# Optimization experiments

Measured on AMD Instinct MI355X. Metric: run time of the kernel, lower is better.

The kernel has to match this reference:

```python
import jax, jax.numpy as jnp
import numpy as np

B, N, DIM = 4, 4096, 512
HEADS, DH = 8, 64          # dim_head = dim // 8
M = 256                    # num_landmarks = dim // 2
ITERS = 6                  # pinv iterations
K = 33                     # residual depthwise conv kernel
INNER = HEADS * DH


def setup_inputs() -> dict:
    key = jax.random.key(0)
    ks = jax.random.split(key, 7)
    return {
        "x": jax.random.normal(ks[0], (B, N, DIM), jnp.float32),
        "norm_w": 1.0 + 0.02 * jax.random.normal(ks[1], (DIM,), jnp.float32),
        "norm_b": 0.02 * jax.random.normal(ks[2], (DIM,), jnp.float32),
        "w_qkv": jax.random.normal(ks[3], (DIM, 3 * INNER), jnp.float32) / np.sqrt(DIM),
        "w_out": jax.random.normal(ks[4], (INNER, DIM), jnp.float32) / np.sqrt(INNER),
        "b_out": 0.02 * jax.random.normal(ks[5], (DIM,), jnp.float32),
        "res_w": jax.random.normal(ks[6], (HEADS, 1, K, 1), jnp.float32) / np.sqrt(K),
    }


def _moore_penrose_pinv(x, iters):
    # iterative Newton-Schulz pseudoinverse, as in lucidrains nystrom-attention
    abs_x = jnp.abs(x)
    col = abs_x.sum(-1)
    row = abs_x.sum(-2)
    z = jnp.swapaxes(x, -1, -2) / (jnp.max(col) * jnp.max(row))
    I = jnp.eye(x.shape[-1], dtype=x.dtype)
    for _ in range(iters):
        xz = x @ z
        z = 0.25 * z @ (13.0 * I - xz @ (15.0 * I - xz @ (7.0 * I - xz)))
    return z


def reference(x, norm_w, norm_b, w_qkv, w_out, b_out, res_w):
    # LayerNorm (eps=1e-5, torch default)
    mu = x.mean(-1, keepdims=True)
    var = ((x - mu) ** 2).mean(-1, keepdims=True)
    xn = (x - mu) / jnp.sqrt(var + 1e-5) * norm_w + norm_b

    qkv = xn @ w_qkv                               # [B,N,3*INNER]
    q, k, v = jnp.split(qkv, 3, axis=-1)
    to_heads = lambda t: t.reshape(B, N, HEADS, DH).transpose(0, 2, 1, 3)  # [B,H,N,D]
    q, k, v = to_heads(q), to_heads(k), to_heads(v)
    q = q * (DH ** -0.5)

    # landmarks: mean over consecutive blocks of l = N // M tokens
    l = N // M
    q_l = q.reshape(B, HEADS, M, l, DH).mean(3)    # [B,H,M,D]
    k_l = k.reshape(B, HEADS, M, l, DH).mean(3)

    sim1 = jnp.einsum('bhid,bhjd->bhij', q, k_l)   # [B,H,N,M]
    sim2 = jnp.einsum('bhid,bhjd->bhij', q_l, k_l) # [B,H,M,M]
    sim3 = jnp.einsum('bhid,bhjd->bhij', q_l, k)   # [B,H,M,N]
    a1 = jax.nn.softmax(sim1, -1)
    a2 = jax.nn.softmax(sim2, -1)
    a3 = jax.nn.softmax(sim3, -1)

    a2_inv = _moore_penrose_pinv(a2, ITERS)
    out = (a1 @ a2_inv) @ (a3 @ v)                 # [B,H,N,D]

    # residual depthwise conv over sequence dim (Conv2d(h,h,(33,1),groups=h))
    out = out + jax.lax.conv_general_dilated(
        v, res_w, (1, 1), ((K // 2, K // 2), (0, 0)),
        feature_group_count=HEADS,
        dimension_numbers=('NCHW', 'OIHW', 'NCHW'))

    out = out.transpose(0, 2, 1, 3).reshape(B, N, INNER)
    out = out @ w_out + b_out                      # to_out (dropout inactive at eval)
    return x + out                                 # TransLayer residual
```

## Files before the change

kernel.cpp:

```cpp
#include <hip/hip_runtime.h>
#include <math.h>

typedef unsigned short u16;
typedef short s16x8 __attribute__((ext_vector_type(8)));
typedef float f32x4 __attribute__((ext_vector_type(4)));

#define MFMA16(a, b, c) __builtin_amdgcn_mfma_f32_16x16x32_bf16((a), (b), (c), 0, 0, 0)

__device__ __forceinline__ u16 f2b(float f) {
  unsigned u = __float_as_uint(f);
  unsigned r = (u + 0x7fff + ((u >> 16) & 1)) >> 16;
  return (u16)r;
}
__device__ __forceinline__ float b2f(u16 h) { return __uint_as_float(((unsigned)h) << 16); }

__global__ __launch_bounds__(256) void prep_kernel(const float* __restrict__ x, const float* __restrict__ w,
    const float* __restrict__ b, u16* __restrict__ xn,
    const float* __restrict__ Wq, u16* __restrict__ WqT,
    const float* __restrict__ Wo, u16* __restrict__ WoT,
    unsigned* __restrict__ scal) {
  int bI = blockIdx.x;
  int t = threadIdx.x;
  if (bI == 0 && t == 0) { scal[0] = 0u; scal[1] = 0u; }
  if (bI < 16384) {
    int row = bI;
    const float* xr = x + (size_t)row * 512;
    float v0 = xr[t], v1 = xr[t + 256];
    float s = v0 + v1, ss = v0*v0 + v1*v1;
    for (int o = 32; o > 0; o >>= 1) { s += __shfl_down(s, o); ss += __shfl_down(ss, o); }
    __shared__ float ls[4], lss[4];
    int wid = t >> 6, lane = t & 63;
    if (lane == 0) { ls[wid] = s; lss[wid] = ss; }
    __syncthreads();
    float tot  = ls[0]+ls[1]+ls[2]+ls[3];
    float tot2 = lss[0]+lss[1]+lss[2]+lss[3];
    float mean = tot * (1.f/512);
    float var  = tot2 * (1.f/512) - mean*mean;
    float inv = rsqrtf(var + 1e-5f);
    u16* xo = xn + (size_t)row * 512;
    xo[t]     = f2b((v0-mean)*inv*w[t]     + b[t]);
    xo[t+256] = f2b((v1-mean)*inv*w[t+256] + b[t+256]);
  } else if (bI < 16384 + 3072) {
    int idx = (bI - 16384)*256 + t;
    int r = idx / 1536, c = idx - r*1536;
    WqT[(size_t)c*512 + r] = f2b(Wq[idx]);
  } else {
    int idx = (bI - 19456)*256 + t;
    int r = idx >> 9, c = idx & 511;
    WoT[(size_t)c*512 + r] = f2b(Wo[idx]);
  }
}

__global__ __launch_bounds__(256) void vtrans(const u16* __restrict__ v, u16* __restrict__ vT) {
  __shared__ u16 tile[64][72];
  int bh = blockIdx.y, n0 = blockIdx.x * 64;
  int t = threadIdx.x;
  const u16* vb = v + ((size_t)bh*4096 + n0)*64;
  #pragma unroll
  for (int p = 0; p < 2; p++) {
    int c = t + p*256;
    int r = c >> 3, col = (c & 7)*8;
    *(uint4*)&tile[r][col] = *(const uint4*)&vb[(size_t)r*64 + col];
  }
  __syncthreads();
  #pragma unroll
  for (int p = 0; p < 2; p++) {
    int c = t + p*256;
    int d = c >> 3, ncol = (c & 7)*8;
    u16 tmp[8];
    #pragma unroll
    for (int j = 0; j < 8; j++) tmp[j] = tile[ncol + j][d];
    *(uint4*)&vT[((size_t)bh*64 + d)*4096 + n0 + ncol] = *(uint4*)tmp;
  }
}

__device__ __forceinline__ void gemm128_pf(const u16* __restrict__ A, const u16* __restrict__ BT,
    int K, int ldA, int ldBT, int row0, int col0, u16* As, u16* Bs, f32x4 acc[4][4]) {
  int t = threadIdx.x, lane = t & 63, wid = t >> 6;
  int wr = (wid >> 1) * 64, wc = (wid & 1) * 64;
  int lr = lane & 15, lg = lane >> 4;
  int sr = t >> 2, sc = (t & 3) * 8;
  const u16* Ar0 = A  + (size_t)(row0 + sr)*ldA + sc;
  const u16* Ar1 = A  + (size_t)(row0 + sr + 64)*ldA + sc;
  const u16* Br0 = BT + (size_t)(col0 + sr)*ldBT + sc;
  const u16* Br1 = BT + (size_t)(col0 + sr + 64)*ldBT + sc;
  uint4 pa0 = *(const uint4*)Ar0, pa1 = *(const uint4*)Ar1;
  uint4 pb0 = *(const uint4*)Br0, pb1 = *(const uint4*)Br1;
  for (int k0 = 0; k0 < K; k0 += 32) {
    __syncthreads();
    *(uint4*)&As[sr*40 + sc]        = pa0;
    *(uint4*)&As[(sr + 64)*40 + sc] = pa1;
    *(uint4*)&Bs[sr*40 + sc]        = pb0;
    *(uint4*)&Bs[(sr + 64)*40 + sc] = pb1;
    __syncthreads();
    if (k0 + 32 < K) {
      pa0 = *(const uint4*)(Ar0 + k0 + 32);
      pa1 = *(const uint4*)(Ar1 + k0 + 32);
      pb0 = *(const uint4*)(Br0 + k0 + 32);
      pb1 = *(const uint4*)(Br1 + k0 + 32);
    }
    s16x8 af[4], bf[4];
    #pragma unroll
    for (int f = 0; f < 4; f++) {
      af[f] = *(s16x8*)&As[(wr + f*16 + lr)*40 + lg*8];
      bf[f] = *(s16x8*)&Bs[(wc + f*16 + lr)*40 + lg*8];
    }
    #pragma unroll
    for (int i = 0; i < 4; i++)
// ... 96 lines not shown
          if (part == 0) ql[dst] = f2b(s * (0.125f/16.f));
          else           kl[dst] = f2b(s * (1.f/16.f));
        }
      }
    }
  }
}

__global__ __launch_bounds__(256, 4) void out_mfma(const u16* __restrict__ outh, const u16* __restrict__ wT,
    const float* __restrict__ bo, const float* __restrict__ x, float* __restrict__ out) {
  __shared__ u16 As[128*40], Bs[128*40];
  f32x4 acc[4][4];
  #pragma unroll
  for (int i = 0; i < 4; i++)
    #pragma unroll
    for (int j = 0; j < 4; j++) acc[i][j] = (f32x4)0.f;
  int bI = blockIdx.x;
  int job = (bI & 7)*64 + (bI >> 3);
  int row0 = (job / 4) * 128, col0 = (job % 4) * 128;
  gemm128_pf(outh, wT, 512, 512, 512, row0, col0, As, Bs, acc);
  int t = threadIdx.x, lane = t & 63, wid = t >> 6, lr = lane & 15, lg = lane >> 4;
  int wr = (wid >> 1)*64, wc = (wid & 1)*64;
  #pragma unroll
  for (int i = 0; i < 4; i++)
    #pragma unroll
    for (int j = 0; j < 4; j++)
      #pragma unroll
      for (int r = 0; r < 4; r++) {
        int row = row0 + wr + i*16 + lg*4 + r;
        int col = col0 + wc + j*16 + lr;
        size_t idx = (size_t)row*512 + col;
        out[idx] = x[idx] + acc[i][j][r] + bo[col];
      }
}

__global__ __launch_bounds__(256) void pinv_s1(const u16* __restrict__ a2h, const u16* __restrict__ zcT,
    u16* __restrict__ xz, u16* __restrict__ xzT, u16* __restrict__ e1T) {
  __shared__ u16 As[64*72], Bs[64*72];
  size_t bb = (size_t)blockIdx.z << 16;
  f32x4 acc[2][2];
  #pragma unroll
  for (int i = 0; i < 2; i++) { acc[i][0] = (f32x4)0.f; acc[i][1] = (f32x4)0.f; }
  int row0 = blockIdx.y*64, col0 = blockIdx.x*64;
  gemm64_pf(a2h + bb, zcT + bb, row0, col0, As, Bs, acc);
  int t = threadIdx.x, lane = t & 63, wid = t >> 6, lr = lane & 15, lg = lane >> 4;
  int wr = (wid >> 1)*32, wc = (wid & 1)*32;
  #pragma unroll
  for (int i = 0; i < 2; i++)
    #pragma unroll
    for (int j = 0; j < 2; j++)
      #pragma unroll
      for (int r = 0; r < 4; r++) {
        int row = row0 + wr + i*16 + lg*4 + r;
        int col = col0 + wc + j*16 + lr;
        float c = acc[i][j][r];
        xz [bb + (size_t)row*256 + col] = f2b(c);
        xzT[bb + (size_t)col*256 + row] = f2b(c);
        e1T[bb + (size_t)col*256 + row] = f2b((row == col ? 7.f : 0.f) - c);
      }
}

__global__ __launch_bounds__(256) void pinv_s2(const u16* __restrict__ xz, const u16* __restrict__ e1T,
    const u16* __restrict__ zc, const u16* __restrict__ xzT,
    u16* __restrict__ e2T, u16* __restrict__ W) {
  __shared__ u16 As[64*72], Bs[64*72];
  int bz = blockIdx.z;
// ... 71 lines not shown
    __syncthreads();
    *(uint4*)&As[sr*40 + sc] = pa;
    *(uint4*)&Bs[sr*40 + sc] = pb;
    __syncthreads();
    if (k0 + 32 < K) {
      pa = *(const uint4*)(Arow + k0 + 32);
      pb = *(const uint4*)(Brow + k0 + 32);
    }
    s16x8 af[2], bf[2];
    #pragma unroll
    for (int f = 0; f < 2; f++) {
      af[f] = *(s16x8*)&As[(wr + f*16 + lr)*40 + lg*8];
      bf[f] = *(s16x8*)&Bs[(wc + f*16 + lr)*40 + lg*8];
    }
    #pragma unroll
    for (int i = 0; i < 2; i++)
      #pragma unroll
      for (int j = 0; j < 2; j++)
        acc[i][j] = MFMA16(af[i], bf[j], acc[i][j]);
  }
  size_t cb = (size_t)batch*M*N;
  #pragma unroll
  for (int i = 0; i < 2; i++)
    #pragma unroll
    for (int j = 0; j < 2; j++)
      #pragma unroll
      for (int r = 0; r < 4; r++) {
        int row = row0 + wr + i*16 + lg*4 + r;
        int col = col0 + wc + j*16 + lr;
        CT[cb + (size_t)col*M + row] = f2b(acc[i][j][r]);
      }
}

__global__ __launch_bounds__(256, 4) void sim2_mfma(const u16* __restrict__ ql, const u16* __restrict__ kl,
    float* __restrict__ a2, u16* __restrict__ a2h, float* __restrict__ pcs) {
  __shared__ u16 Qs[64*72];
  __shared__ u16 Ks2[256*72];
  __shared__ float wcol[4*256];
  int rq = blockIdx.x, bh = blockIdx.y;
  int t = threadIdx.x, lane = t & 63, wid = t >> 6, lr = lane & 15, lg = lane >> 4;
  #pragma unroll
  for (int p = 0; p < 2; p++) {
    int c = t + p*256;
    int r = c >> 3, col = (c & 7)*8;
    *(uint4*)&Qs[r*72 + col] = *(const uint4*)&ql[((size_t)bh*256 + rq*64 + r)*64 + col];
  }
  #pragma unroll
  for (int p = 0; p < 8; p++) {
    int c = t + p*256;
    int r = c >> 3, col = (c & 7)*8;
    *(uint4*)&Ks2[r*72 + col] = *(const uint4*)&kl[((size_t)bh*256 + r)*64 + col];
  }
  __syncthreads();
  float colp[16];
  #pragma unroll
  for (int cf = 0; cf < 16; cf++) colp[cf] = 0.f;
  int rbase = wid*16;
  s16x8 a0 = *(s16x8*)&Qs[(rbase + lr)*72 + lg*8];
  s16x8 a1 = *(s16x8*)&Qs[(rbase + lr)*72 + 32 + lg*8];
  f32x4 sf[16];
  #pragma unroll
  for (int cf = 0; cf < 16; cf++) {
    s16x8 b0 = *(s16x8*)&Ks2[(cf*16 + lr)*72 + lg*8];
    s16x8 b1 = *(s16x8*)&Ks2[(cf*16 + lr)*72 + 32 + lg*8];
    sf[cf] = MFMA16(a1, b1, MFMA16(a0, b0, (f32x4)0.f));
  }
  #pragma unroll
  for (int r = 0; r < 4; r++) {
    float mx = -3e38f;
    #pragma unroll
    for (int cf = 0; cf < 16; cf++) mx = fmaxf(mx, sf[cf][r]);
    #pragma unroll
    for (int o = 1; o < 16; o <<= 1) mx = fmaxf(mx, __shfl_xor(mx, o));
    float sum = 0.f;
    #pragma unroll
    for (int cf = 0; cf < 16; cf++) { sf[cf][r] = __expf(sf[cf][r] - mx); sum += sf[cf][r]; }
    #pragma unroll
    for (int o = 1; o < 16; o <<= 1) sum += __shfl_xor(sum, o);
    float inv = 1.f / sum;
    int row = rq*64 + rbase + lg*4 + r;
    size_t base = (size_t)bh*65536 + (size_t)row*256;
    #pragma unroll
    for (int cf = 0; cf < 16; cf++) {
      float pp = sf[cf][r] * inv;
      a2[base + cf*16 + lr] = pp;
      a2h[base + cf*16 + lr] = f2b(pp);
      colp[cf] += pp;
    }
  }
  #pragma unroll
  for (int cf = 0; cf < 16; cf++) {
    colp[cf] += __shfl_xor(colp[cf], 16);
    colp[cf] += __shfl_xor(colp[cf], 32);
  }
  if (lg == 0) {
    #pragma unroll
    for (int cf = 0; cf < 16; cf++) wcol[wid*256 + cf*16 + lr] = colp[cf];
  }
  __syncthreads();
  pcs[((size_t)bh*4 + rq)*256 + t] = wcol[t] + wcol[256 + t] + wcol[512 + t] + wcol[768 + t];
}

__global__ __launch_bounds__(256) void colmax_kernel(const float* __restrict__ pcs, unsigned* __restrict__ scal) {
  __shared__ float red[256];
  int bh = blockIdx.x, t = threadIdx.x;
  size_t b4 = (size_t)bh*4*256;
  red[t] = pcs[b4 + t] + pcs[b4 + 256 + t] + pcs[b4 + 512 + t] + pcs[b4 + 768 + t];
  __syncthreads();
  for (int o = 128; o > 0; o >>= 1) {
    if (t < o) red[t] = fmaxf(red[t], red[t+o]);
    __syncthreads();
  }
  if (t == 0) atomicMax(scal + 1, __float_as_uint(red[0]));
}

__global__ __launch_bounds__(256) void flash_part(const u16* __restrict__ Q, const u16* __restrict__ Kg,
    const u16* __restrict__ VT, u16* __restrict__ po, float* __restrict__ pl) {
  __shared__ u16 Ks[64*72];
  __shared__ u16 Vs[64*72];
  __shared__ u16 Ps[4*16*72];
  int ch = blockIdx.x, qg = blockIdx.y, bh = blockIdx.z;
  int t = threadIdx.x, lane = t & 63, wid = t >> 6, lr = lane & 15, lg = lane >> 4;
  const u16* Qb  = Q  + ((size_t)bh*256)*64;
  const u16* Kb  = Kg + ((size_t)bh*4096 + ch*512)*64;
  const u16* VTb = VT + ((size_t)bh*64)*4096 + ch*512;
  s16x8 aq[2][2];
  #pragma unroll
  for (int qq = 0; qq < 2; qq++) {
    int qrow = (qg*2 + qq)*64 + wid*16 + lr;
    aq[qq][0] = *(const s16x8*)&Qb[(size_t)qrow*64 + lg*8];
    aq[qq][1] = *(const s16x8*)&Qb[(size_t)qrow*64 + 32 + lg*8];
  }
  f32x4 oacc[2][4];
  f32x4 lacc[2];
  #pragma unroll
  for (int qq = 0; qq < 2; qq++) {
    lacc[qq] = (f32x4)0.f;
    #pragma unroll
    for (int f = 0; f < 4; f++) oacc[qq][f] = (f32x4)0.f;
  }
  u16* Pw = Ps + wid*16*72;
  uint4 pk[2], pv[2];
  #pragma unroll
  for (int p = 0; p < 2; p++) {
    int c = t + p*256; int r = c >> 3, cc = (c & 7)*8;
    pk[p] = *(const uint4*)&Kb[(size_t)r*64 + cc];
    pv[p] = *(const uint4*)&VTb[(size_t)r*4096 + cc];
  }
  for (int k0 = 0; k0 < 512; k0 += 64) {
    __syncthreads();
    #pragma unroll
    for (int p = 0; p < 2; p++) {
      int c = t + p*256; int r = c >> 3, cc = (c & 7)*8;
      *(uint4*)&Ks[r*72 + cc] = pk[p];
      *(uint4*)&Vs[r*72 + cc] = pv[p];
    }
    __syncthreads();
    if (k0 + 64 < 512) {
      #pragma unroll
      for (int p = 0; p < 2; p++) {
        int c = t + p*256; int r = c >> 3, cc = (c & 7)*8;
        pk[p] = *(const uint4*)&Kb[(size_t)(k0 + 64 + r)*64 + cc];
        pv[p] = *(const uint4*)&VTb[(size_t)r*4096 + k0 + 64 + cc];
      }
    }
    #pragma unroll
    for (int qq = 0; qq < 2; qq++) {
      f32x4 sf[4];
      #pragma unroll
      for (int f = 0; f < 4; f++) {
        s16x8 b0 = *(s16x8*)&Ks[(f*16 + lr)*72 + lg*8];
        s16x8 b1 = *(s16x8*)&Ks[(f*16 + lr)*72 + 32 + lg*8];
        f32x4 s = (f32x4)0.f;
        s = MFMA16(aq[qq][0], b0, s);
        s = MFMA16(aq[qq][1], b1, s);
        sf[f] = s;
      }
      #pragma unroll
      for (int r = 0; r < 4; r++) {
        #pragma unroll
        for (int f = 0; f < 4; f++) {
          float pv2 = __expf(sf[f][r] - 8.f);
          lacc[qq][r] += pv2;
          Pw[(lg*4 + r)*72 + f*16 + lr] = f2b(pv2);
        }
      }
      #pragma unroll
      for (int ks = 0; ks < 2; ks++) {
        s16x8 ap = *(s16x8*)&Pw[lr*72 + ks*32 + lg*8];
        #pragma unroll
        for (int df = 0; df < 4; df++) {
          s16x8 bv = *(s16x8*)&Vs[(df*16 + lr)*72 + ks*32 + lg*8];
          oacc[qq][df] = MFMA16(ap, bv, oacc[qq][df]);
        }
      }
    }
  }
  #pragma unroll
  for (int qq = 0; qq < 2; qq++) {
    #pragma unroll
    for (int r = 0; r < 4; r++) {
      float s = lacc[qq][r];
      #pragma unroll
      for (int o = 1; o < 16; o <<= 1) s += __shfl_xor(s, o);
      lacc[qq][r] = s;
    }
  }
  #pragma unroll
  for (int qq = 0; qq < 2; qq++) {
    int pidx = (bh*4 + qg*2 + qq)*8 + ch;
    #pragma unroll
    for (int r = 0; r < 4; r++) {
      int lrow = wid*16 + lg*4 + r;
      if (lr == 0) pl[pidx*64 + lrow] = lacc[qq][r];
      uint2 pw2;
      pw2.x = (unsigned)f2b(oacc[qq][0][r]) | ((unsigned)f2b(oacc[qq][1][r]) << 16);
      pw2.y = (unsigned)f2b(oacc[qq][2][r]) | ((unsigned)f2b(oacc[qq][3][r]) << 16);
      *(uint2*)&po[((size_t)pidx*64 + lrow)*64 + lr*4] = pw2;
    }
  }
}

__global__ __launch_bounds__(256) void merge_z0(const u16* __restrict__ po,
    const float* __restrict__ pl, u16* __restrict__ a3vT,
    const float* __restrict__ a2, const unsigned* __restrict__ scal,
    u16* __restrict__ zA, u16* __restrict__ zAT) {
  __shared__ u16 tile[64*72];
  int bI = blockIdx.x;
  int t = threadIdx.x;
  if (bI < 128) {
    int qt = bI & 3, bh = bI >> 2;
    int lrow = t & 63, dg = t >> 6;
    int pbase = (bh*4 + qt)*8;
    float L = 0.f;
    #pragma unroll
    for (int ch = 0; ch < 8; ch++) L += pl[(pbase+ch)*64 + lrow];
    float Oacc[16];
    #pragma unroll
    for (int ss = 0; ss < 16; ss++) Oacc[ss] = 0.f;
    #pragma unroll
    for (int ch = 0; ch < 8; ch++) {
      const u16* pr = &po[(((size_t)(pbase+ch)*64 + lrow)*64) + dg*16];
      uint4 v0 = *(const uint4*)pr;
      uint4 v1 = *(const uint4*)(pr + 8);
      unsigned arr[8] = {v0.x, v0.y, v0.z, v0.w, v1.x, v1.y, v1.z, v1.w};
      #pragma unroll
      for (int jj = 0; jj < 8; jj++) {
        Oacc[jj*2]   += b2f((u16)(arr[jj] & 0xffff));
        Oacc[jj*2+1] += b2f((u16)(arr[jj] >> 16));
      }
    }
    float Linv = 1.f / L;
    #pragma unroll
    for (int ss = 0; ss < 16; ss++) {
      int s = dg*16 + ss;
      int c = ((s & 3) << 4) | (s >> 2);
      tile[c*72 + lrow] = f2b(Oacc[ss] * Linv);
    }
    __syncthreads();
    #pragma unroll
    for (int p = 0; p < 2; p++) {
      int idx = t + p*256;
      int d = idx >> 3, seg = idx & 7;
      u16 tmp[8];
      #pragma unroll
      for (int j = 0; j < 8; j++) tmp[j] = tile[d*72 + seg*8 + j];
      *(uint4*)&a3vT[((size_t)bh*64 + d)*256 + qt*64 + seg*8] = *(uint4*)tmp;
    }
  } else {
    size_t idx = (size_t)(bI - 128)*256 + t;
    float inv = 1.f / __uint_as_float(scal[1]);
    size_t bh = idx >> 16; int rem = (int)(idx & 65535); int i = rem >> 8, j = rem & 255;
    zA[idx]  = f2b(a2[(bh<<16) + ((size_t)j<<8) + i] * inv);
    zAT[idx] = f2b(a2[idx] * inv);
  }
}

__global__ __launch_bounds__(256, 4) void flash_a1(const u16* __restrict__ Q, const u16* __restrict__ Kl,
    const u16* __restrict__ W2T, u16* __restrict__ outh) {
  __shared__ u16 Ks[64*72];
  __shared__ u16 Vs[64*264];
  __shared__ u16 Ps[4*16*264];
  int bh = blockIdx.y;
  int q0 = blockIdx.x * 64;
  int t = threadIdx.x, lane = t & 63, wid = t >> 6, lr = lane & 15, lg = lane >> 4;
  const u16* Qb = Q + ((size_t)bh*4096)*64;
  #pragma unroll
  for (int p = 0; p < 8; p++) {
    int c = t + p*256; int r = c >> 5, col = (c & 31)*8;
    *(uint4*)&Vs[r*264 + col] = *(const uint4*)&W2T[((size_t)bh*64 + r)*256 + col];
  }
  int qrow = q0 + wid*16 + lr;
  s16x8 aq0 = *(const s16x8*)&Qb[(size_t)qrow*64 + lg*8];
  s16x8 aq1 = *(const s16x8*)&Qb[(size_t)qrow*64 + 32 + lg*8];
  f32x4 sf[16];
  #pragma unroll
  for (int f = 0; f < 16; f++) sf[f] = (f32x4)0.f;
  #pragma unroll
  for (int kt = 0; kt < 4; kt++) {
    __syncthreads();
    #pragma unroll
    for (int p = 0; p < 2; p++) {
      int c = t + p*256; int r = c >> 3, cc = (c & 7)*8;
      *(uint4*)&Ks[r*72 + cc] = *(const uint4*)&Kl[((size_t)bh*256 + kt*64 + r)*64 + cc];
    }
    __syncthreads();
    #pragma unroll
    for (int f2 = 0; f2 < 4; f2++) {
      s16x8 b0 = *(s16x8*)&Ks[(f2*16 + lr)*72 + lg*8];
      s16x8 b1 = *(s16x8*)&Ks[(f2*16 + lr)*72 + 32 + lg*8];
// ... 4 lines not shown
  float linv[4];
  #pragma unroll
  for (int r = 0; r < 4; r++) {
    float sum = 0.f;
    #pragma unroll
    for (int f = 0; f < 16; f++) {
      float pv = __expf(sf[f][r] - 8.f);
      sum += pv;
      Pw[(lg*4 + r)*264 + f*16 + lr] = f2b(pv);
    }
    #pragma unroll
    for (int o = 1; o < 16; o <<= 1) sum += __shfl_xor(sum, o);
    linv[r] = 1.f / sum;
  }
  f32x4 oacc[4];
  #pragma unroll
  for (int f = 0; f < 4; f++) oacc[f] = (f32x4)0.f;
  #pragma unroll
  for (int ks = 0; ks < 8; ks++) {
    s16x8 ap = *(s16x8*)&Pw[lr*264 + ks*32 + lg*8];
    #pragma unroll
    for (int df = 0; df < 4; df++) {
      s16x8 bv = *(s16x8*)&Vs[(df*16 + lr)*264 + ks*32 + lg*8];
      oacc[df] = MFMA16(ap, bv, oacc[df]);
    }
  }
  int b = bh >> 3, h = bh & 7;
  #pragma unroll
  for (int df = 0; df < 4; df++)
    #pragma unroll
    for (int r = 0; r < 4; r++) {
      int lrow = wid*16 + lg*4 + r;
      int col = df*16 + lr;
      outh[((size_t)(b*4096 + q0 + lrow))*512 + h*64 + col] = f2b(oacc[df][r] * linv[r]);
    }
}

__global__ __launch_bounds__(256) void conv_lds(const u16* __restrict__ v, const float* __restrict__ rw,
                                                u16* __restrict__ outh) {
  __shared__ u16 tile[160*72];
  __shared__ float wsm[33];
  int bh = blockIdx.y;
  int n0 = blockIdx.x * 128;
  int b = bh >> 3, h = bh & 7;
  int t = threadIdx.x;
  if (t < 33) wsm[t] = rw[h*33 + t];
  const u16* vb = v + ((size_t)bh*4096)*64;
  #pragma unroll
  for (int p = 0; p < 5; p++) {
    int c = t + p*256;
    int r = c >> 3, col = (c & 7)*8;
    int nn = n0 - 16 + r;
    uint4 val = make_uint4(0u,0u,0u,0u);
    if (nn >= 0 && nn < 4096) val = *(const uint4*)&vb[(size_t)nn*64 + col];
    *(uint4*)&tile[r*72 + col] = val;
  }
  __syncthreads();
  int d8 = (t & 7) * 8;
  int r0 = t >> 3;
  #pragma unroll
  for (int pass = 0; pass < 4; pass++) {
    int lrow = pass*32 + r0;
    float acc[8] = {};
    #pragma unroll
    for (int j = 0; j < 33; j++) {
      uint4 vv = *(uint4*)&tile[(lrow + j)*72 + d8];
      float w = wsm[j];
      acc[0] += b2f((u16)(vv.x & 0xffff)) * w;
      acc[1] += b2f((u16)(vv.x >> 16))    * w;
      acc[2] += b2f((u16)(vv.y & 0xffff)) * w;
      acc[3] += b2f((u16)(vv.y >> 16))    * w;
      acc[4] += b2f((u16)(vv.z & 0xffff)) * w;
      acc[5] += b2f((u16)(vv.z >> 16))    * w;
      acc[6] += b2f((u16)(vv.w & 0xffff)) * w;
      acc[7] += b2f((u16)(vv.w >> 16))    * w;
    }
    size_t oi = ((size_t)(b*4096 + n0 + lrow))*512 + h*64 + d8;
    uint4 ov = *(uint4*)&outh[oi];
    uint4 nv;
    nv.x = (unsigned)f2b(b2f((u16)(ov.x & 0xffff)) + acc[0]) | ((unsigned)f2b(b2f((u16)(ov.x >> 16)) + acc[1]) << 16);
    nv.y = (unsigned)f2b(b2f((u16)(ov.y & 0xffff)) + acc[2]) | ((unsigned)f2b(b2f((u16)(ov.y >> 16)) + acc[3]) << 16);
    nv.z = (unsigned)f2b(b2f((u16)(ov.z & 0xffff)) + acc[4]) | ((unsigned)f2b(b2f((u16)(ov.z >> 16)) + acc[5]) << 16);
    nv.w = (unsigned)f2b(b2f((u16)(ov.w & 0xffff)) + acc[6]) | ((unsigned)f2b(b2f((u16)(ov.w >> 16)) + acc[7]) << 16);
    *(uint4*)&outh[oi] = nv;
  }
}

extern "C" void kernel_launch(void* const* d_in, const int* in_sizes, int n_in,
                              void* d_out, int out_size, void* d_ws, size_t ws_size,
                              hipStream_t stream) {
  const float* x      = (const float*)d_in[0];
  const float* norm_w = (const float*)d_in[1];
  const float* norm_b = (const float*)d_in[2];
  const float* w_qkv  = (const float*)d_in[3];
  const float* w_out  = (const float*)d_in[4];
  const float* b_out  = (const float*)d_in[5];
  const float* res_w  = (const float*)d_in[6];
  float* out = (float*)d_out;
  char* ws = (char*)d_ws;

  size_t off = 0;
  u16* xn    = (u16*)(ws + off); off += 16777216;
  u16* q     = (u16*)(ws + off); off += 16777216;
  u16* k     = (u16*)(ws + off); off += 16777216;
  u16* v     = (u16*)(ws + off); off += 16777216;
  u16* vT    = (u16*)(ws + off); off += 16777216;
  u16* ql    = (u16*)(ws + off); off += 1048576;
  u16* kl    = (u16*)(ws + off); off += 1048576;
  float* a2  = (float*)(ws + off); off += 8388608;
  u16* a2h   = (u16*)(ws + off); off += 4194304;
  u16* zA    = (u16*)(ws + off); off += 4194304;
  u16* zAT   = (u16*)(ws + off); off += 4194304;
  u16* zB    = (u16*)(ws + off); off += 4194304;
  u16* zBT   = (u16*)(ws + off); off += 4194304;
  u16* xz    = (u16*)(ws + off); off += 4194304;
  u16* xzT   = (u16*)(ws + off); off += 4194304;
  u16* e1T   = (u16*)(ws + off); off += 4194304;
  u16* e2T   = (u16*)(ws + off); off += 4194304;
  u16* Wm    = (u16*)(ws + off); off += 4194304;
  u16* a3vT  = (u16*)(ws + off); off += 1048576;
  u16* w2T   = (u16*)(ws + off); off += 1048576;
  u16* wqkvT = (u16*)(ws + off); off += 1572864;
  u16* woutT = (u16*)(ws + off); off += 524288;
  u16* outh  = (u16*)(ws + off); off += 16777216;
  u16* po    = (u16*)(ws + off); off += 8388608;
  float* pl  = (float*)(ws + off); off += 262144;
  float* pcs = (float*)(ws + off); off += 131072;
  unsigned* scal = (unsigned*)(ws + off); off += 8;

  prep_kernel<<<20480, 256, 0, stream>>>(x, norm_w, norm_b, xn, w_qkv, wqkvT, w_out, woutT, scal);
  qkv_mfma<<<1536, 256, 0, stream>>>(xn, wqkvT, q, k, v, ql, kl);
  vtrans<<<dim3(64, 32), 256, 0, stream>>>(v, vT);
  sim2_mfma<<<dim3(4, 32), 256, 0, stream>>>(ql, kl, a2, a2h, pcs);
  colmax_kernel<<<32, 256, 0, stream>>>(pcs, scal);
  flash_part<<<dim3(8, 2, 32), 256, 0, stream>>>(ql, k, vT, po, pl);
  merge_z0<<<8320, 256, 0, stream>>>(po, pl, a3vT, a2, scal, zA, zAT);

  u16 *zc = zA, *zcT = zAT, *zn = zB, *znT = zBT;
  for (int it = 0; it < 6; it++) {
    pinv_s1<<<dim3(4,4,32), 256, 0, stream>>>(a2h, zcT, xz, xzT, e1T);
    pinv_s2<<<dim3(4,4,64), 256, 0, stream>>>(xz, e1T, zc, xzT, e2T, Wm);
    pinv_s3<<<dim3(4,4,32), 256, 0, stream>>>(Wm, e2T, zc, zn, znT);
    u16* tp;
    tp = zc; zc = zn; zn = tp;
    tp = zcT; zcT = znT; znT = tp;
  }

  bmm64<<<dim3(1,4,32), 256, 0, stream>>>(zc, a3vT, w2T, 256, 64, 256);
  flash_a1<<<dim3(64, 32), 256, 0, stream>>>(q, kl, w2T, outh);
  conv_lds<<<dim3(32, 32), 256, 0, stream>>>(v, res_w, outh);
  out_mfma<<<512, 256, 0, stream>>>(outh, woutT, b_out, x, out);
}
```

Measured before the change: 397.6 us.

## Fuse vtrans, sim2 softmax and residual conv into one mid kernel

Three independent stages (landmark softmax sim2, V transpose, depthwise residual conv) now run as one kernel, with each block choosing its task from the block index. The conv result is written to outh first, and flash_a1 adds its attention output on top by read-modify-write, so the separate conv pass that reread outh goes away. The fp32 a2 buffer is removed and merge_z0 builds z0 from the bf16 a2h instead. This saves launches and memory traffic, at the cost of a slightly less precise initial z.

```diff
diff --git a/kernel.cpp b/kernel.cpp
--- a/kernel.cpp
+++ b/kernel.cpp
@@ -51,29 +51,6 @@
   }
 }
 
-__global__ __launch_bounds__(256) void vtrans(const u16* __restrict__ v, u16* __restrict__ vT) {
-  __shared__ u16 tile[64][72];
-  int bh = blockIdx.y, n0 = blockIdx.x * 64;
-  int t = threadIdx.x;
-  const u16* vb = v + ((size_t)bh*4096 + n0)*64;
-  #pragma unroll
-  for (int p = 0; p < 2; p++) {
-    int c = t + p*256;
-    int r = c >> 3, col = (c & 7)*8;
-    *(uint4*)&tile[r][col] = *(const uint4*)&vb[(size_t)r*64 + col];
-  }
-  __syncthreads();
-  #pragma unroll
-  for (int p = 0; p < 2; p++) {
-    int c = t + p*256;
-    int d = c >> 3, ncol = (c & 7)*8;
-    u16 tmp[8];
-    #pragma unroll
-    for (int j = 0; j < 8; j++) tmp[j] = tile[ncol + j][d];
-    *(uint4*)&vT[((size_t)bh*64 + d)*4096 + n0 + ncol] = *(uint4*)tmp;
-  }
-}
-
 __device__ __forceinline__ void gemm128_pf(const u16* __restrict__ A, const u16* __restrict__ BT,
     int K, int ldA, int ldBT, int row0, int col0, u16* As, u16* Bs, f32x4 acc[4][4]) {
   int t = threadIdx.x, lane = t & 63, wid = t >> 6;
@@ -236,6 +213,323 @@
         size_t idx = (size_t)row*512 + col;
         out[idx] = x[idx] + acc[i][j][r] + bo[col];
       }
+}
+
+__global__ __launch_bounds__(256) void mid_kernel(
+    const u16* __restrict__ v, u16* __restrict__ vT,
+    const u16* __restrict__ ql, const u16* __restrict__ kl,
+    u16* __restrict__ a2h, float* __restrict__ pcs,
+    const float* __restrict__ rw, u16* __restrict__ outh) {
+  __shared__ __align__(16) u16 smem[25600];
+  int bI = blockIdx.x;
+  int t = threadIdx.x;
+  if (bI < 128) {
+    int rq = bI & 3, bh = bI >> 2;
+    u16* Qs  = smem;
+    u16* Ks2 = smem + 4608;
+    float* wcol = (float*)(smem + 23040);
+    int lane = t & 63, wid = t >> 6, lr = lane & 15, lg = lane >> 4;
+    #pragma unroll
+    for (int p = 0; p < 2; p++) {
+      int c = t + p*256;
+      int r = c >> 3, col = (c & 7)*8;
+      *(uint4*)&Qs[r*72 + col] = *(const uint4*)&ql[((size_t)bh*256 + rq*64 + r)*64 + col];
+    }
+    #pragma unroll
+    for (int p = 0; p < 8; p++) {
+      int c = t + p*256;
+      int r = c >> 3, col = (c & 7)*8;
+      *(uint4*)&Ks2[r*72 + col] = *(const uint4*)&kl[((size_t)bh*256 + r)*64 + col];
+    }
+    __syncthreads();
+    float colp[16];
+    #pragma unroll
+    for (int cf = 0; cf < 16; cf++) colp[cf] = 0.f;
+    int rbase = wid*16;
+    s16x8 a0 = *(s16x8*)&Qs[(rbase + lr)*72 + lg*8];
+    s16x8 a1 = *(s16x8*)&Qs[(rbase + lr)*72 + 32 + lg*8];
+    f32x4 sf[16];
+    #pragma unroll
+    for (int cf = 0; cf < 16; cf++) {
+      s16x8 b0 = *(s16x8*)&Ks2[(cf*16 + lr)*72 + lg*8];
+      s16x8 b1 = *(s16x8*)&Ks2[(cf*16 + lr)*72 + 32 + lg*8];
+      sf[cf] = MFMA16(a1, b1, MFMA16(a0, b0, (f32x4)0.f));
+    }
+    #pragma unroll
+    for (int r = 0; r < 4; r++) {
+      float mx = -3e38f;
+      #pragma unroll
+      for (int cf = 0; cf < 16; cf++) mx = fmaxf(mx, sf[cf][r]);
+      #pragma unroll
+      for (int o = 1; o < 16; o <<= 1) mx = fmaxf(mx, __shfl_xor(mx, o));
+      float sum = 0.f;
+      #pragma unroll
+      for (int cf = 0; cf < 16; cf++) { sf[cf][r] = __expf(sf[cf][r] - mx); sum += sf[cf][r]; }
+      #pragma unroll
+      for (int o = 1; o < 16; o <<= 1) sum += __shfl_xor(sum, o);
+      float inv = 1.f / sum;
+      int row = rq*64 + rbase + lg*4 + r;
+      size_t base = (size_t)bh*65536 + (size_t)row*256;
+      #pragma unroll
+      for (int cf = 0; cf < 16; cf++) {
+        float pp = sf[cf][r] * inv;
+        a2h[base + cf*16 + lr] = f2b(pp);
+        colp[cf] += pp;
+      }
+    }
+    #pragma unroll
+    for (int cf = 0; cf < 16; cf++) {
+      colp[cf] += __shfl_xor(colp[cf], 16);
+      colp[cf] += __shfl_xor(colp[cf], 32);
+    }
+    if (lg == 0) {
+      #pragma unroll
+      for (int cf = 0; cf < 16; cf++) wcol[wid*256 + cf*16 + lr] = colp[cf];
+    }
+    __syncthreads();
+    pcs[((size_t)bh*4 + rq)*256 + t] = wcol[t] + wcol[256 + t] + wcol[512 + t] + wcol[768 + t];
+  } else if (bI < 2176) {
+    int idx = bI - 128;
+    int bh = idx >> 6, n0 = (idx & 63) * 64;
+    u16* tile = smem;
+    const u16* vb = v + ((size_t)bh*4096 + n0)*64;
+    #pragma unroll
+    for (int p = 0; p < 2; p++) {
+      int c = t + p*256;
+      int r = c >> 3, col = (c & 7)*8;
+      *(uint4*)&tile[r*72 + col] = *(const uint4*)&vb[(size_t)r*64 + col];
+    }
+    __syncthreads();
+    #pragma unroll
+    for (int p = 0; p < 2; p++) {
+      int c = t + p*256;
+      int d = c >> 3, ncol = (c & 7)*8;
+      u16 tmp[8];
+      #pragma unroll
+      for (int j = 0; j < 8; j++) tmp[j] = tile[(ncol + j)*72 + d];
+      *(uint4*)&vT[((size_t)bh*64 + d)*4096 + n0 + ncol] = *(uint4*)tmp;
+    }
+  } else {
+    int idx = bI - 2176;
+    int bh = idx >> 5, n0 = (idx & 31) * 128;
+    int b = bh >> 3, h = bh & 7;
+    u16* tile = smem;
+    float* wsm = (float*)(smem + 11520);
+    if (t < 33) wsm[t] = rw[h*33 + t];
+    const u16* vb = v + ((size_t)bh*4096)*64;
+    #pragma unroll
+    for (int p = 0; p < 5; p++) {
+      int c = t + p*256;
+      int r = c >> 3, col = (c & 7)*8;
+      int nn = n0 - 16 + r;
+      uint4 val = make_uint4(0u,0u,0u,0u);
+      if (nn >= 0 && nn < 4096) val = *(const uint4*)&vb[(size_t)nn*64 + col];
+      *(uint4*)&tile[r*72 + col] = val;
+    }
+    __syncthreads();
+    int d8 = (t & 7) * 8;
+    int r0 = t >> 3;
+    #pragma unroll
+    for (int pass = 0; pass < 4; pass++) {
+      int lrow = pass*32 + r0;
+      float acc[8] = {};
+      #pragma unroll
+      for (int j = 0; j < 33; j++) {
+        uint4 vv = *(uint4*)&tile[(lrow + j)*72 + d8];
+        float w = wsm[j];
+        acc[0] += b2f((u16)(vv.x & 0xffff)) * w;
+        acc[1] += b2f((u16)(vv.x >> 16))    * w;
+        acc[2] += b2f((u16)(vv.y & 0xffff)) * w;
+        acc[3] += b2f((u16)(vv.y >> 16))    * w;
+        acc[4] += b2f((u16)(vv.z & 0xffff)) * w;
+        acc[5] += b2f((u16)(vv.z >> 16))    * w;
+        acc[6] += b2f((u16)(vv.w & 0xffff)) * w;
+        acc[7] += b2f((u16)(vv.w >> 16))    * w;
+      }
+      size_t oi = ((size_t)(b*4096 + n0 + lrow))*512 + h*64 + d8;
+      uint4 nv;
+      nv.x = (unsigned)f2b(acc[0]) | ((unsigned)f2b(acc[1]) << 16);
+      nv.y = (unsigned)f2b(acc[2]) | ((unsigned)f2b(acc[3]) << 16);
+      nv.z = (unsigned)f2b(acc[4]) | ((unsigned)f2b(acc[5]) << 16);
+      nv.w = (unsigned)f2b(acc[6]) | ((unsigned)f2b(acc[7]) << 16);
+      *(uint4*)&outh[oi] = nv;
+    }
+  }
+}
+
+__global__ __launch_bounds__(256) void colmax_kernel(const float* __restrict__ pcs, unsigned* __restrict__ scal) {
+  __shared__ float red[256];
+  int bh = blockIdx.x, t = threadIdx.x;
+  size_t b4 = (size_t)bh*4*256;
+  red[t] = pcs[b4 + t] + pcs[b4 + 256 + t] + pcs[b4 + 512 + t] + pcs[b4 + 768 + t];
+  __syncthreads();
+  for (int o = 128; o > 0; o >>= 1) {
+    if (t < o) red[t] = fmaxf(red[t], red[t+o]);
+    __syncthreads();
+  }
+  if (t == 0) atomicMax(scal + 1, __float_as_uint(red[0]));
+}
+
+__global__ __launch_bounds__(256) void flash_part(const u16* __restrict__ Q, const u16* __restrict__ Kg,
+    const u16* __restrict__ VT, u16* __restrict__ po, float* __restrict__ pl) {
+  __shared__ u16 Ks[64*72];
+  __shared__ u16 Vs[64*72];
+  __shared__ u16 Ps[4*16*72];
+  int ch = blockIdx.x, qg = blockIdx.y, bh = blockIdx.z;
+  int t = threadIdx.x, lane = t & 63, wid = t >> 6, lr = lane & 15, lg = lane >> 4;
+  const u16* Qb  = Q  + ((size_t)bh*256)*64;
+  const u16* Kb  = Kg + ((size_t)bh*4096 + ch*512)*64;
+  const u16* VTb = VT + ((size_t)bh*64)*4096 + ch*512;
+  s16x8 aq[2][2];
+  #pragma unroll
+  for (int qq = 0; qq < 2; qq++) {
+    int qrow = (qg*2 + qq)*64 + wid*16 + lr;
+    aq[qq][0] = *(const s16x8*)&Qb[(size_t)qrow*64 + lg*8];
+    aq[qq][1] = *(const s16x8*)&Qb[(size_t)qrow*64 + 32 + lg*8];
+  }
+  f32x4 oacc[2][4];
+  f32x4 lacc[2];
+  #pragma unroll
+  for (int qq = 0; qq < 2; qq++) {
+    lacc[qq] = (f32x4)0.f;
+    #pragma unroll
+    for (int f = 0; f < 4; f++) oacc[qq][f] = (f32x4)0.f;
+  }
+  u16* Pw = Ps + wid*16*72;
+  uint4 pk[2], pv[2];
+  #pragma unroll
+  for (int p = 0; p < 2; p++) {
+    int c = t + p*256; int r = c >> 3, cc = (c & 7)*8;
+    pk[p] = *(const uint4*)&Kb[(size_t)r*64 + cc];
+    pv[p] = *(const uint4*)&VTb[(size_t)r*4096 + cc];
+  }
+  for (int k0 = 0; k0 < 512; k0 += 64) {
+    __syncthreads();
+    #pragma unroll
+    for (int p = 0; p < 2; p++) {
+      int c = t + p*256; int r = c >> 3, cc = (c & 7)*8;
+      *(uint4*)&Ks[r*72 + cc] = pk[p];
+      *(uint4*)&Vs[r*72 + cc] = pv[p];
+    }
+    __syncthreads();
+    if (k0 + 64 < 512) {
+      #pragma unroll
+      for (int p = 0; p < 2; p++) {
+        int c = t + p*256; int r = c >> 3, cc = (c & 7)*8;
+        pk[p] = *(const uint4*)&Kb[(size_t)(k0 + 64 + r)*64 + cc];
+        pv[p] = *(const uint4*)&VTb[(size_t)r*4096 + k0 + 64 + cc];
+      }
+    }
+    #pragma unroll
+    for (int qq = 0; qq < 2; qq++) {
+      f32x4 sf[4];
+      #pragma unroll
+      for (int f = 0; f < 4; f++) {
+        s16x8 b0 = *(s16x8*)&Ks[(f*16 + lr)*72 + lg*8];
+        s16x8 b1 = *(s16x8*)&Ks[(f*16 + lr)*72 + 32 + lg*8];
+        f32x4 s = (f32x4)0.f;
+        s = MFMA16(aq[qq][0], b0, s);
+        s = MFMA16(aq[qq][1], b1, s);
+        sf[f] = s;
+      }
+      #pragma unroll
+      for (int r = 0; r < 4; r++) {
+        #pragma unroll
+        for (int f = 0; f < 4; f++) {
+          float pv2 = __expf(sf[f][r] - 8.f);
+          lacc[qq][r] += pv2;
+          Pw[(lg*4 + r)*72 + f*16 + lr] = f2b(pv2);
+        }
+      }
+      #pragma unroll
+      for (int ks = 0; ks < 2; ks++) {
+        s16x8 ap = *(s16x8*)&Pw[lr*72 + ks*32 + lg*8];
+        #pragma unroll
+        for (int df = 0; df < 4; df++) {
+          s16x8 bv = *(s16x8*)&Vs[(df*16 + lr)*72 + ks*32 + lg*8];
+          oacc[qq][df] = MFMA16(ap, bv, oacc[qq][df]);
+        }
+      }
+    }
+  }
+  #pragma unroll
+  for (int qq = 0; qq < 2; qq++) {
+    #pragma unroll
+    for (int r = 0; r < 4; r++) {
+      float s = lacc[qq][r];
+      #pragma unroll
+      for (int o = 1; o < 16; o <<= 1) s += __shfl_xor(s, o);
+      lacc[qq][r] = s;
+    }
+  }
+  #pragma unroll
+  for (int qq = 0; qq < 2; qq++) {
+    int pidx = (bh*4 + qg*2 + qq)*8 + ch;
+    #pragma unroll
+    for (int r = 0; r < 4; r++) {
+      int lrow = wid*16 + lg*4 + r;
+      if (lr == 0) pl[pidx*64 + lrow] = lacc[qq][r];
+      uint2 pw2;
+      pw2.x = (unsigned)f2b(oacc[qq][0][r]) | ((unsigned)f2b(oacc[qq][1][r]) << 16);
+      pw2.y = (unsigned)f2b(oacc[qq][2][r]) | ((unsigned)f2b(oacc[qq][3][r]) << 16);
+      *(uint2*)&po[((size_t)pidx*64 + lrow)*64 + lr*4] = pw2;
+    }
+  }
+}
+
+__global__ __launch_bounds__(256) void merge_z0(const u16* __restrict__ po,
+    const float* __restrict__ pl, u16* __restrict__ a3vT,
+    const u16* __restrict__ a2h, const unsigned* __restrict__ scal,
+    u16* __restrict__ zA, u16* __restrict__ zAT) {
+  __shared__ u16 tile[64*72];
+  int bI = blockIdx.x;
+  int t = threadIdx.x;
+  if (bI < 128) {
+    int qt = bI & 3, bh = bI >> 2;
+    int lrow = t & 63, dg = t >> 6;
+    int pbase = (bh*4 + qt)*8;
+    float L = 0.f;
+    #pragma unroll
+    for (int ch = 0; ch < 8; ch++) L += pl[(pbase+ch)*64 + lrow];
+    float Oacc[16];
+    #pragma unroll
+    for (int ss = 0; ss < 16; ss++) Oacc[ss] = 0.f;
+    #pragma unroll
+    for (int ch = 0; ch < 8; ch++) {
+      const u16* pr = &po[(((size_t)(pbase+ch)*64 + lrow)*64) + dg*16];
+      uint4 v0 = *(const uint4*)pr;
+      uint4 v1 = *(const uint4*)(pr + 8);
+      unsigned arr[8] = {v0.x, v0.y, v0.z, v0.w, v1.x, v1.y, v1.z, v1.w};
+      #pragma unroll
+      for (int jj = 0; jj < 8; jj++) {
+        Oacc[jj*2]   += b2f((u16)(arr[jj] & 0xffff));
+        Oacc[jj*2+1] += b2f((u16)(arr[jj] >> 16));
+      }
+    }
+    float Linv = 1.f / L;
+    #pragma unroll
+    for (int ss = 0; ss < 16; ss++) {
+      int s = dg*16 + ss;
+      int c = ((s & 3) << 4) | (s >> 2);
+      tile[c*72 + lrow] = f2b(Oacc[ss] * Linv);
+    }
+    __syncthreads();
+    #pragma unroll
+    for (int p = 0; p < 2; p++) {
+      int idx = t + p*256;
+      int d = idx >> 3, seg = idx & 7;
+      u16 tmp[8];
+      #pragma unroll
+      for (int j = 0; j < 8; j++) tmp[j] = tile[d*72 + seg*8 + j];
+      *(uint4*)&a3vT[((size_t)bh*64 + d)*256 + qt*64 + seg*8] = *(uint4*)tmp;
+    }
+  } else {
+    size_t idx = (size_t)(bI - 128)*256 + t;
+    float inv = 1.f / __uint_as_float(scal[1]);
+    size_t bh = idx >> 16; int rem = (int)(idx & 65535); int i = rem >> 8, j = rem & 255;
+    zA[idx]  = f2b(b2f(a2h[(bh<<16) + ((size_t)j<<8) + i]) * inv);
+    zAT[idx] = f2b(b2f(a2h[idx]) * inv);
+  }
 }
 
 __global__ __launch_bounds__(256) void pinv_s1(const u16* __restrict__ a2h, const u16* __restrict__ zcT,
@@ -373,250 +667,6 @@
       }
 }
 
-__global__ __launch_bounds__(256, 4) void sim2_mfma(const u16* __restrict__ ql, const u16* __restrict__ kl,
-    float* __restrict__ a2, u16* __restrict__ a2h, float* __restrict__ pcs) {
-  __shared__ u16 Qs[64*72];
-  __shared__ u16 Ks2[256*72];
-  __shared__ float wcol[4*256];
-  int rq = blockIdx.x, bh = blockIdx.y;
-  int t = threadIdx.x, lane = t & 63, wid = t >> 6, lr = lane & 15, lg = lane >> 4;
-  #pragma unroll
-  for (int p = 0; p < 2; p++) {
-    int c = t + p*256;
-    int r = c >> 3, col = (c & 7)*8;
-    *(uint4*)&Qs[r*72 + col] = *(const uint4*)&ql[((size_t)bh*256 + rq*64 + r)*64 + col];
-  }
-  #pragma unroll
-  for (int p = 0; p < 8; p++) {
-    int c = t + p*256;
-    int r = c >> 3, col = (c & 7)*8;
-    *(uint4*)&Ks2[r*72 + col] = *(const uint4*)&kl[((size_t)bh*256 + r)*64 + col];
-  }
-  __syncthreads();
-  float colp[16];
-  #pragma unroll
-  for (int cf = 0; cf < 16; cf++) colp[cf] = 0.f;
-  int rbase = wid*16;
-  s16x8 a0 = *(s16x8*)&Qs[(rbase + lr)*72 + lg*8];
-  s16x8 a1 = *(s16x8*)&Qs[(rbase + lr)*72 + 32 + lg*8];
-  f32x4 sf[16];
-  #pragma unroll
-  for (int cf = 0; cf < 16; cf++) {
-    s16x8 b0 = *(s16x8*)&Ks2[(cf*16 + lr)*72 + lg*8];
-    s16x8 b1 = *(s16x8*)&Ks2[(cf*16 + lr)*72 + 32 + lg*8];
-    sf[cf] = MFMA16(a1, b1, MFMA16(a0, b0, (f32x4)0.f));
-  }
-  #pragma unroll
-  for (int r = 0; r < 4; r++) {
-    float mx = -3e38f;
-    #pragma unroll
-    for (int cf = 0; cf < 16; cf++) mx = fmaxf(mx, sf[cf][r]);
-    #pragma unroll
-    for (int o = 1; o < 16; o <<= 1) mx = fmaxf(mx, __shfl_xor(mx, o));
-    float sum = 0.f;
-    #pragma unroll
-    for (int cf = 0; cf < 16; cf++) { sf[cf][r] = __expf(sf[cf][r] - mx); sum += sf[cf][r]; }
-    #pragma unroll
-    for (int o = 1; o < 16; o <<= 1) sum += __shfl_xor(sum, o);
-    float inv = 1.f / sum;
-    int row = rq*64 + rbase + lg*4 + r;
-    size_t base = (size_t)bh*65536 + (size_t)row*256;
-    #pragma unroll
-    for (int cf = 0; cf < 16; cf++) {
-      float pp = sf[cf][r] * inv;
-      a2[base + cf*16 + lr] = pp;
-      a2h[base + cf*16 + lr] = f2b(pp);
-      colp[cf] += pp;
-    }
-  }
-  #pragma unroll
-  for (int cf = 0; cf < 16; cf++) {
-    colp[cf] += __shfl_xor(colp[cf], 16);
-    colp[cf] += __shfl_xor(colp[cf], 32);
-  }
-  if (lg == 0) {
-    #pragma unroll
-    for (int cf = 0; cf < 16; cf++) wcol[wid*256 + cf*16 + lr] = colp[cf];
-  }
-  __syncthreads();
-  pcs[((size_t)bh*4 + rq)*256 + t] = wcol[t] + wcol[256 + t] + wcol[512 + t] + wcol[768 + t];
-}
-
-__global__ __launch_bounds__(256) void colmax_kernel(const float* __restrict__ pcs, unsigned* __restrict__ scal) {
-  __shared__ float red[256];
-  int bh = blockIdx.x, t = threadIdx.x;
-  size_t b4 = (size_t)bh*4*256;
-  red[t] = pcs[b4 + t] + pcs[b4 + 256 + t] + pcs[b4 + 512 + t] + pcs[b4 + 768 + t];
-  __syncthreads();
-  for (int o = 128; o > 0; o >>= 1) {
-    if (t < o) red[t] = fmaxf(red[t], red[t+o]);
-    __syncthreads();
-  }
-  if (t == 0) atomicMax(scal + 1, __float_as_uint(red[0]));
-}
-
-__global__ __launch_bounds__(256) void flash_part(const u16* __restrict__ Q, const u16* __restrict__ Kg,
-    const u16* __restrict__ VT, u16* __restrict__ po, float* __restrict__ pl) {
-  __shared__ u16 Ks[64*72];
-  __shared__ u16 Vs[64*72];
-  __shared__ u16 Ps[4*16*72];
-  int ch = blockIdx.x, qg = blockIdx.y, bh = blockIdx.z;
-  int t = threadIdx.x, lane = t & 63, wid = t >> 6, lr = lane & 15, lg = lane >> 4;
-  const u16* Qb  = Q  + ((size_t)bh*256)*64;
-  const u16* Kb  = Kg + ((size_t)bh*4096 + ch*512)*64;
-  const u16* VTb = VT + ((size_t)bh*64)*4096 + ch*512;
-  s16x8 aq[2][2];
-  #pragma unroll
-  for (int qq = 0; qq < 2; qq++) {
-    int qrow = (qg*2 + qq)*64 + wid*16 + lr;
-    aq[qq][0] = *(const s16x8*)&Qb[(size_t)qrow*64 + lg*8];
-    aq[qq][1] = *(const s16x8*)&Qb[(size_t)qrow*64 + 32 + lg*8];
-  }
-  f32x4 oacc[2][4];
-  f32x4 lacc[2];
-  #pragma unroll
-  for (int qq = 0; qq < 2; qq++) {
-    lacc[qq] = (f32x4)0.f;
-    #pragma unroll
-    for (int f = 0; f < 4; f++) oacc[qq][f] = (f32x4)0.f;
-  }
-  u16* Pw = Ps + wid*16*72;
-  uint4 pk[2], pv[2];
-  #pragma unroll
-  for (int p = 0; p < 2; p++) {
-    int c = t + p*256; int r = c >> 3, cc = (c & 7)*8;
-    pk[p] = *(const uint4*)&Kb[(size_t)r*64 + cc];
-    pv[p] = *(const uint4*)&VTb[(size_t)r*4096 + cc];
-  }
-  for (int k0 = 0; k0 < 512; k0 += 64) {
-    __syncthreads();
-    #pragma unroll
-    for (int p = 0; p < 2; p++) {
-      int c = t + p*256; int r = c >> 3, cc = (c & 7)*8;
-      *(uint4*)&Ks[r*72 + cc] = pk[p];
-      *(uint4*)&Vs[r*72 + cc] = pv[p];
-    }
-    __syncthreads();
-    if (k0 + 64 < 512) {
-      #pragma unroll
-      for (int p = 0; p < 2; p++) {
-        int c = t + p*256; int r = c >> 3, cc = (c & 7)*8;
-        pk[p] = *(const uint4*)&Kb[(size_t)(k0 + 64 + r)*64 + cc];
-        pv[p] = *(const uint4*)&VTb[(size_t)r*4096 + k0 + 64 + cc];
-      }
-    }
-    #pragma unroll
-    for (int qq = 0; qq < 2; qq++) {
-      f32x4 sf[4];
-      #pragma unroll
-      for (int f = 0; f < 4; f++) {
-        s16x8 b0 = *(s16x8*)&Ks[(f*16 + lr)*72 + lg*8];
-        s16x8 b1 = *(s16x8*)&Ks[(f*16 + lr)*72 + 32 + lg*8];
-        f32x4 s = (f32x4)0.f;
-        s = MFMA16(aq[qq][0], b0, s);
-        s = MFMA16(aq[qq][1], b1, s);
-        sf[f] = s;
-      }
-      #pragma unroll
-      for (int r = 0; r < 4; r++) {
-        #pragma unroll
-        for (int f = 0; f < 4; f++) {
-          float pv2 = __expf(sf[f][r] - 8.f);
-          lacc[qq][r] += pv2;
-          Pw[(lg*4 + r)*72 + f*16 + lr] = f2b(pv2);
-        }
-      }
-      #pragma unroll
-      for (int ks = 0; ks < 2; ks++) {
-        s16x8 ap = *(s16x8*)&Pw[lr*72 + ks*32 + lg*8];
-        #pragma unroll
-        for (int df = 0; df < 4; df++) {
-          s16x8 bv = *(s16x8*)&Vs[(df*16 + lr)*72 + ks*32 + lg*8];
-          oacc[qq][df] = MFMA16(ap, bv, oacc[qq][df]);
-        }
-      }
-    }
-  }
-  #pragma unroll
-  for (int qq = 0; qq < 2; qq++) {
-    #pragma unroll
-    for (int r = 0; r < 4; r++) {
-      float s = lacc[qq][r];
-      #pragma unroll
-      for (int o = 1; o < 16; o <<= 1) s += __shfl_xor(s, o);
-      lacc[qq][r] = s;
-    }
-  }
-  #pragma unroll
-  for (int qq = 0; qq < 2; qq++) {
-    int pidx = (bh*4 + qg*2 + qq)*8 + ch;
-    #pragma unroll
-    for (int r = 0; r < 4; r++) {
-      int lrow = wid*16 + lg*4 + r;
-      if (lr == 0) pl[pidx*64 + lrow] = lacc[qq][r];
-      uint2 pw2;
-      pw2.x = (unsigned)f2b(oacc[qq][0][r]) | ((unsigned)f2b(oacc[qq][1][r]) << 16);
-      pw2.y = (unsigned)f2b(oacc[qq][2][r]) | ((unsigned)f2b(oacc[qq][3][r]) << 16);
-      *(uint2*)&po[((size_t)pidx*64 + lrow)*64 + lr*4] = pw2;
-    }
-  }
-}
-
-__global__ __launch_bounds__(256) void merge_z0(const u16* __restrict__ po,
-    const float* __restrict__ pl, u16* __restrict__ a3vT,
-    const float* __restrict__ a2, const unsigned* __restrict__ scal,
-    u16* __restrict__ zA, u16* __restrict__ zAT) {
-  __shared__ u16 tile[64*72];
-  int bI = blockIdx.x;
-  int t = threadIdx.x;
-  if (bI < 128) {
-    int qt = bI & 3, bh = bI >> 2;
-    int lrow = t & 63, dg = t >> 6;
-    int pbase = (bh*4 + qt)*8;
-    float L = 0.f;
-    #pragma unroll
-    for (int ch = 0; ch < 8; ch++) L += pl[(pbase+ch)*64 + lrow];
-    float Oacc[16];
-    #pragma unroll
-    for (int ss = 0; ss < 16; ss++) Oacc[ss] = 0.f;
-    #pragma unroll
-    for (int ch = 0; ch < 8; ch++) {
-      const u16* pr = &po[(((size_t)(pbase+ch)*64 + lrow)*64) + dg*16];
-      uint4 v0 = *(const uint4*)pr;
-      uint4 v1 = *(const uint4*)(pr + 8);
-      unsigned arr[8] = {v0.x, v0.y, v0.z, v0.w, v1.x, v1.y, v1.z, v1.w};
-      #pragma unroll
-      for (int jj = 0; jj < 8; jj++) {
-        Oacc[jj*2]   += b2f((u16)(arr[jj] & 0xffff));
-        Oacc[jj*2+1] += b2f((u16)(arr[jj] >> 16));
-      }
-    }
-    float Linv = 1.f / L;
-    #pragma unroll
-    for (int ss = 0; ss < 16; ss++) {
-      int s = dg*16 + ss;
-      int c = ((s & 3) << 4) | (s >> 2);
-      tile[c*72 + lrow] = f2b(Oacc[ss] * Linv);
-    }
-    __syncthreads();
-    #pragma unroll
-    for (int p = 0; p < 2; p++) {
-      int idx = t + p*256;
-      int d = idx >> 3, seg = idx & 7;
-      u16 tmp[8];
-      #pragma unroll
-      for (int j = 0; j < 8; j++) tmp[j] = tile[d*72 + seg*8 + j];
-      *(uint4*)&a3vT[((size_t)bh*64 + d)*256 + qt*64 + seg*8] = *(uint4*)tmp;
-    }
-  } else {
-    size_t idx = (size_t)(bI - 128)*256 + t;
-    float inv = 1.f / __uint_as_float(scal[1]);
-    size_t bh = idx >> 16; int rem = (int)(idx & 65535); int i = rem >> 8, j = rem & 255;
-    zA[idx]  = f2b(a2[(bh<<16) + ((size_t)j<<8) + i] * inv);
-    zAT[idx] = f2b(a2[idx] * inv);
-  }
-}
-
 __global__ __launch_bounds__(256, 4) void flash_a1(const u16* __restrict__ Q, const u16* __restrict__ Kl,
     const u16* __restrict__ W2T, u16* __restrict__ outh) {
   __shared__ u16 Ks[64*72];
@@ -687,58 +737,9 @@
     for (int r = 0; r < 4; r++) {
       int lrow = wid*16 + lg*4 + r;
       int col = df*16 + lr;
-      outh[((size_t)(b*4096 + q0 + lrow))*512 + h*64 + col] = f2b(oacc[df][r] * linv[r]);
-    }
-}
-
-__global__ __launch_bounds__(256) void conv_lds(const u16* __restrict__ v, const float* __restrict__ rw,
-                                                u16* __restrict__ outh) {
-  __shared__ u16 tile[160*72];
-  __shared__ float wsm[33];
-  int bh = blockIdx.y;
-  int n0 = blockIdx.x * 128;
-  int b = bh >> 3, h = bh & 7;
-  int t = threadIdx.x;
-  if (t < 33) wsm[t] = rw[h*33 + t];
-  const u16* vb = v + ((size_t)bh*4096)*64;
-  #pragma unroll
-  for (int p = 0; p < 5; p++) {
-    int c = t + p*256;
-    int r = c >> 3, col = (c & 7)*8;
-    int nn = n0 - 16 + r;
-    uint4 val = make_uint4(0u,0u,0u,0u);
-    if (nn >= 0 && nn < 4096) val = *(const uint4*)&vb[(size_t)nn*64 + col];
-    *(uint4*)&tile[r*72 + col] = val;
-  }
-  __syncthreads();
-  int d8 = (t & 7) * 8;
-  int r0 = t >> 3;
-  #pragma unroll
-  for (int pass = 0; pass < 4; pass++) {
-    int lrow = pass*32 + r0;
-    float acc[8] = {};
-    #pragma unroll
-    for (int j = 0; j < 33; j++) {
-      uint4 vv = *(uint4*)&tile[(lrow + j)*72 + d8];
-      float w = wsm[j];
-      acc[0] += b2f((u16)(vv.x & 0xffff)) * w;
-      acc[1] += b2f((u16)(vv.x >> 16))    * w;
-      acc[2] += b2f((u16)(vv.y & 0xffff)) * w;
-      acc[3] += b2f((u16)(vv.y >> 16))    * w;
-      acc[4] += b2f((u16)(vv.z & 0xffff)) * w;
-      acc[5] += b2f((u16)(vv.z >> 16))    * w;
-      acc[6] += b2f((u16)(vv.w & 0xffff)) * w;
-      acc[7] += b2f((u16)(vv.w >> 16))    * w;
-    }
-    size_t oi = ((size_t)(b*4096 + n0 + lrow))*512 + h*64 + d8;
-    uint4 ov = *(uint4*)&outh[oi];
-    uint4 nv;
-    nv.x = (unsigned)f2b(b2f((u16)(ov.x & 0xffff)) + acc[0]) | ((unsigned)f2b(b2f((u16)(ov.x >> 16)) + acc[1]) << 16);
-    nv.y = (unsigned)f2b(b2f((u16)(ov.y & 0xffff)) + acc[2]) | ((unsigned)f2b(b2f((u16)(ov.y >> 16)) + acc[3]) << 16);
-    nv.z = (unsigned)f2b(b2f((u16)(ov.z & 0xffff)) + acc[4]) | ((unsigned)f2b(b2f((u16)(ov.z >> 16)) + acc[5]) << 16);
-    nv.w = (unsigned)f2b(b2f((u16)(ov.w & 0xffff)) + acc[6]) | ((unsigned)f2b(b2f((u16)(ov.w >> 16)) + acc[7]) << 16);
-    *(uint4*)&outh[oi] = nv;
-  }
+      size_t oi = ((size_t)(b*4096 + q0 + lrow))*512 + h*64 + col;
+      outh[oi] = f2b(b2f(outh[oi]) + oacc[df][r] * linv[r]);
+    }
 }
 
 extern "C" void kernel_launch(void* const* d_in, const int* in_sizes, int n_in,
@@ -762,7 +763,6 @@
   u16* vT    = (u16*)(ws + off); off += 16777216;
   u16* ql    = (u16*)(ws + off); off += 1048576;
   u16* kl    = (u16*)(ws + off); off += 1048576;
-  float* a2  = (float*)(ws + off); off += 8388608;
   u16* a2h   = (u16*)(ws + off); off += 4194304;
   u16* zA    = (u16*)(ws + off); off += 4194304;
   u16* zAT   = (u16*)(ws + off); off += 4194304;
@@ -785,11 +785,10 @@
 
   prep_kernel<<<20480, 256, 0, stream>>>(x, norm_w, norm_b, xn, w_qkv, wqkvT, w_out, woutT, scal);
   qkv_mfma<<<1536, 256, 0, stream>>>(xn, wqkvT, q, k, v, ql, kl);
-  vtrans<<<dim3(64, 32), 256, 0, stream>>>(v, vT);
-  sim2_mfma<<<dim3(4, 32), 256, 0, stream>>>(ql, kl, a2, a2h, pcs);
+  mid_kernel<<<3200, 256, 0, stream>>>(v, vT, ql, kl, a2h, pcs, res_w, outh);
   colmax_kernel<<<32, 256, 0, stream>>>(pcs, scal);
   flash_part<<<dim3(8, 2, 32), 256, 0, stream>>>(ql, k, vT, po, pl);
-  merge_z0<<<8320, 256, 0, stream>>>(po, pl, a3vT, a2, scal, zA, zAT);
+  merge_z0<<<8320, 256, 0, stream>>>(po, pl, a3vT, a2h, scal, zA, zAT);
 
   u16 *zc = zA, *zcT = zAT, *zn = zB, *znT = zBT;
   for (int it = 0; it < 6; it++) {
@@ -803,6 +802,5 @@
 
   bmm64<<<dim3(1,4,32), 256, 0, stream>>>(zc, a3vT, w2T, 256, 64, 256);
   flash_a1<<<dim3(64, 32), 256, 0, stream>>>(q, kl, w2T, outh);
-  conv_lds<<<dim3(32, 32), 256, 0, stream>>>(v, res_w, outh);
   out_mfma<<<512, 256, 0, stream>>>(outh, woutT, b_out, x, out);
 }
```

New measurement: 384.5 us. -3.3%, faster.
